# Kernel tuning notes

Hardware: AMD Instinct MI355X
Metric: run time of the kernel (lower is better)

Reference implementation:

```python
import jax, jax.numpy as jnp
import numpy as np
from jax import lax

C_OUT = 32   # out_capsules[0]
D_OUT = 8    # out_capsules[1]
ROUTING_ITERS = 3
EPS = 1e-8


def squash(s):
    # squash over capsule-channel axis c (dim 1 of B c d h w)
    n2 = jnp.sum(s * s, axis=1, keepdims=True)
    return s * (n2 / (1.0 + n2)) / jnp.sqrt(n2 + EPS)


def setup_inputs() -> dict:
    key = jax.random.key(0)
    k1, k2 = jax.random.split(key)
    x = jax.random.normal(k1, (8, 16, 8, 96, 96), dtype=jnp.float32)
    # torch Conv3d weight layout: (out_ch, in_ch, kD, kH, kW); scaled ~ kaiming-ish
    w_conv = jax.random.normal(k2, (C_OUT * D_OUT, 16, 1, 3, 3), dtype=jnp.float32) * 0.05
    return {"x": x, "w_conv": w_conv}


def reference(x, w_conv):
    # Conv3d, no bias, valid padding, stride 1, kernel (1,3,3)
    u = lax.conv_general_dilated(
        x, w_conv, window_strides=(1, 1, 1), padding='VALID',
        dimension_numbers=('NCDHW', 'OIDHW', 'NCDHW'))  # (B, c*d, D, h, w)
    B, _, D, h, w = u.shape
    # rearrange 'B (c d) D h w -> B c D d h w'
    u = u.reshape(B, C_OUT, D_OUT, D, h, w).transpose(0, 1, 3, 2, 4, 5)

    b = jnp.zeros((B, D, D_OUT, h, w), dtype=u.dtype)
    s = None
    for _ in range(ROUTING_ITERS):
        # softmax_3d: exp normalized over (d, h, w), keeping D
        e = jnp.exp(b)
        c = e / jnp.sum(e, axis=(2, 3, 4), keepdims=True)
        s = jnp.einsum('BDdhw,BcDdhw->Bcdhw', c, u)
        b = b + jnp.einsum('BcDdhw,Bcdhw->BDdhw', u, squash(s))
    return s
```

## Files before the change

### kernel.cpp

```cpp
#include <hip/hip_runtime.h>
#include <math.h>

#define CIN   16
#define DDEP  8
#define HIN   96
#define WIN   96
#define HOUT  94
#define WOUT  94
#define HW    (HOUT*WOUT)
#define CH    256
#define DCAP  8
#define KTOT  (CIN*9)
#define KTILES 5
#define APAD  168
#define EPSQ  1e-8f

#define B_ELEMS ((size_t)8*DDEP*DCAP*HW)
#define WFRAG_ELEMS ((size_t)KTILES*16*64*8)
#define BLK_PER_B (94*12)
#define NBLK ((size_t)8*BLK_PER_B)
#define A_TILE_BYTES ((size_t)64*APAD*2)
#define A_TILE_V4 (A_TILE_BYTES/16)
#define AC_BYTES (NBLK*A_TILE_BYTES)

typedef __attribute__((ext_vector_type(8))) short bf16x8;
typedef __attribute__((ext_vector_type(4))) float f32x4;

__device__ __forceinline__ ushort f2bf(float f) {
    unsigned u = __float_as_uint(f);
    return (ushort)((u + 0x7FFFu + ((u >> 16) & 1u)) >> 16);
}
__device__ __forceinline__ float bf2f(ushort h) {
    return __uint_as_float(((unsigned)h) << 16);
}

__global__ __launch_bounds__(64) void build_wfrag(
    const float* __restrict__ w, ushort* __restrict__ w_hi, ushort* __restrict__ w_lo)
{
    const int lane = threadIdx.x;
    const int nt = blockIdx.x, kt = blockIdx.y;
    const int n  = nt*16 + (lane & 15);
    const int kb = kt*32 + (lane >> 4)*8;
    size_t off = (((size_t)kt*16 + nt)*64 + lane)*8;
    for (int j = 0; j < 8; ++j) {
        int k = kb + j;
        float v = (k < KTOT) ? w[(size_t)n*KTOT + k] : 0.f;
        ushort hi = f2bf(v);
        float  r  = v - bf2f(hi);
        ushort lo = f2bf(r);
        w_hi[off + j] = hi; w_lo[off + j] = lo;
    }
}

__global__ __launch_bounds__(256) void zreduce(
    const float* __restrict__ Zp, float* __restrict__ Z, int dst)
{
    const int bd = blockIdx.x;
    const float* p = Zp + (size_t)bd * BLK_PER_B;
    float s = 0.f;
    for (int i = threadIdx.x; i < BLK_PER_B; i += 256) s += p[i];
    #pragma unroll
    for (int off = 1; off < 64; off <<= 1) s += __shfl_xor(s, off);
    __shared__ float ps[4];
    if ((threadIdx.x & 63) == 0) ps[threadIdx.x >> 6] = s;
    __syncthreads();
    if (threadIdx.x == 0) Z[dst + bd] = ps[0] + ps[1] + ps[2] + ps[3];
}

template<int MODE>
__device__ __forceinline__ void routing_epilogue(
    const f32x4 (&acc)[4][4], const int t, const int wx, const int h0, const int bb,
    const float (*cms)[8], const float* invZ,
    float (*n2s)[8][8], float (*dbs)[8][8][8], float (*sout)[8],
    float* __restrict__ bws, float* __restrict__ Zp, float* __restrict__ out)
{
    const int w0 = wx*8;
    const int wv = t >> 6, lane = t & 63;
    const int m16 = lane & 15, quad = lane >> 4;
    const int d   = m16 & 7;
    const int Dq  = quad >> 1;
    const int wih = quad & 1;

    float svv[4][4];
    {
        float cmw[4][4];
        if (MODE == 0) {
            const float inv = 1.0f / (float)(DCAP * HW);
            #pragma unroll
            for (int mt = 0; mt < 4; ++mt)
                #pragma unroll
                for (int r = 0; r < 4; ++r) cmw[mt][r] = inv;
        } else {
            #pragma unroll
            for (int mt = 0; mt < 4; ++mt) {
                int D = mt*2 + Dq;
                float iz = invZ[D];
                #pragma unroll
                for (int r = 0; r < 4; ++r) cmw[mt][r] = cms[D*8 + d][wih*4 + r] * iz;
            }
        }
        #pragma unroll
        for (int nt = 0; nt < 4; ++nt)
            #pragma unroll
            for (int r = 0; r < 4; ++r) {
                float partial = 0.f;
                #pragma unroll
                for (int mt = 0; mt < 4; ++mt) partial += cmw[mt][r]*acc[mt][nt][r];
                partial += __shfl_xor(partial, 32);
                svv[nt][r] = partial;
            }
    }

    if (MODE == 2) {
        if (quad < 2) {
            #pragma unroll
            for (int nt = 0; nt < 4; ++nt) {
                int ch = wv*64 + nt*16 + m16;
                #pragma unroll
                for (int r = 0; r < 4; ++r) sout[ch][wih*4 + r] = svv[nt][r];
            }
        }
        __syncthreads();
        for (int i = t; i < 1024; i += 256) {
            int c2 = i >> 2, wip = i & 3;
            int w = w0 + wip*2;
            if (w + 1 < WOUT) {
                float2 v2 = { sout[c2][wip*2], sout[c2][wip*2 + 1] };
                *(float2*)&out[((size_t)bb*CH + c2)*HW + (size_t)h0*WOUT + w] = v2;
            }
        }
        return;
    }

    float p2[4];
    #pragma unroll
    for (int r = 0; r < 4; ++r) {
        float s2 = 0.f;
        #pragma unroll
        for (int nt = 0; nt < 4; ++nt) s2 += svv[nt][r]*svv[nt][r];
        p2[r] = s2;
    }
    #pragma unroll
    for (int r = 0; r < 4; ++r) p2[r] += __shfl_xor(p2[r], 8);
    if (quad < 2 && m16 < 8) {
        #pragma unroll
        for (int r = 0; r < 4; ++r) n2s[wv][m16][quad*4 + r] = p2[r];
    }
    __syncthreads();
    float fac[4];
    #pragma unroll
    for (int r = 0; r < 4; ++r) {
        int wi = wih*4 + r;
        float n2 = n2s[0][d][wi] + n2s[1][d][wi] + n2s[2][d][wi] + n2s[3][d][wi];
        fac[r] = (n2 / (1.f + n2)) / sqrtf(n2 + EPSQ);
    }
    float qv[4][4];
    #pragma unroll
    for (int mt = 0; mt < 4; ++mt)
        #pragma unroll
        for (int r = 0; r < 4; ++r) {
            float sum = 0.f;
            #pragma unroll
            for (int nt = 0; nt < 4; ++nt)
                sum += acc[mt][nt][r] * (svv[nt][r] * fac[r]);
            qv[mt][r] = sum;
        }
    #pragma unroll
    for (int mt = 0; mt < 4; ++mt)
        #pragma unroll
        for (int r = 0; r < 4; ++r) qv[mt][r] += __shfl_xor(qv[mt][r], 8);
    if (m16 < 8) {
        #pragma unroll
        for (int mt = 0; mt < 4; ++mt) {
            int D = mt*2 + Dq;
            #pragma unroll
            for (int r = 0; r < 4; ++r) dbs[wv][D][m16][wih*4 + r] = qv[mt][r];
        }
    }
    __syncthreads();
    {
        int Dd = t >> 2, wip = t & 3;
        int D = Dd >> 3, d2 = Dd & 7;
        int w = w0 + wip*2;
        float ez = 0.f;
        if (w + 1 < WOUT) {
            int wi = wip*2;
            float2 add;
            add.x = dbs[0][D][d2][wi]   + dbs[1][D][d2][wi]
                  + dbs[2][D][d2][wi]   + dbs[3][D][d2][wi];
            add.y = dbs[0][D][d2][wi+1] + dbs[1][D][d2][wi+1]
                  + dbs[2][D][d2][wi+1] + dbs[3][D][d2][wi+1];
            float2* bp = (float2*)&bws[((size_t)bb*64 + Dd)*HW + (size_t)h0*WOUT + w];
            if (MODE != 0) { float2 old = *bp; add.x += old.x; add.y += old.y; }
            *bp = add;
            ez = expf(add.x) + expf(add.y);
        }
        #pragma unroll
        for (int off = 1; off < 32; off <<= 1) ez += __shfl_xor(ez, off);
        if ((t & 31) == 0)
            Zp[((size_t)bb*8 + D)*BLK_PER_B + h0*12 + wx] = ez;
    }
}

template<int MODE, int AC>
__global__ __launch_bounds__(256, 2) void conv_mfma_route(
    const float* __restrict__ x,
    const ushort* __restrict__ w_hi, const ushort* __restrict__ w_lo,
    float* __restrict__ bws, const float* __restrict__ Z,
    float* __restrict__ Zp, float* __restrict__ out, float* __restrict__ Ac)
{
    const int t  = threadIdx.x;
    const int wx = blockIdx.x, h0 = blockIdx.y, bb = blockIdx.z;
    const int w0 = wx*8;
    const size_t blk = ((size_t)bb*94 + h0)*12 + wx;

    __shared__ __align__(16) ushort a_hi[64][APAD];
    __shared__ float  cms[64][8];
    __shared__ float  invZ[8];
    __shared__ union {
        float patch[CIN][DDEP][3][10];
        struct { float n2s[4][8][8];
                 float dbs[4][8][8][8]; } ep;
        float sout[256][8];
    } ov;

    if (MODE != 0) {
        if (t < 8) invZ[t] = 1.0f / Z[(MODE == 2 ? 64 : 0) + bb*8 + t];
        for (int v = t; v < 512; v += 256) {
            int Dd = v >> 3, wi = v & 7;
            int w = w0 + wi;
            float bv = (w < WOUT) ? bws[((size_t)bb*64 + Dd)*HW + (size_t)h0*WOUT + w] : 0.f;
            cms[Dd][wi] = expf(bv);
        }
    }

    if (AC == 2) {
        const float4* src = (const float4*)Ac + blk*A_TILE_V4;
        float4* dst = (float4*)&a_hi[0][0];
        for (int i = t; i < A_TILE_V4; i += 256) dst[i] = src[i];
        __syncthreads();
    } else {
        for (int i = t; i < CIN*DDEP*3*10; i += 256) {
            int ci = i / 240, rem = i - ci*240;
            int D  = rem / 30, rem2 = rem - D*30;
            int kh = rem2 / 10, col = rem2 - kh*10;
            int xc = w0 + col; if (xc > 95) xc = 95;
            ov.patch[ci][D][kh][col] =
                x[(((size_t)(bb*CIN + ci)*DDEP + D)*HIN + (h0+kh))*WIN + xc];
        }
        __syncthreads();

        {
            const int site = t >> 2, kg = t & 3;
            const int D = site >> 3, wi = site & 7;
            #pragma unroll
            for (int u2 = 0; u2 < 18; ++u2) {
                int k0 = kg*36 + u2*2;
                int ci0 = k0/9, r0 = k0 - ci0*9, kh0 = r0/3, kw0 = r0 - kh0*3;
                int k1 = k0 + 1;
                int ci1 = k1/9, r1 = k1 - ci1*9, kh1 = r1/3, kw1 = r1 - kh1*3;
                unsigned lo = f2bf(ov.patch[ci0][D][kh0][wi+kw0]);
                unsigned hi = f2bf(ov.patch[ci1][D][kh1][wi+kw1]);
                *(unsigned*)&a_hi[site][k0] = lo | (hi << 16);
            }
            if (t < 64) {
                #pragma unroll
                for (int kk = KTOT; kk < KTILES*32; kk += 2)
                    *(unsigned*)&a_hi[t][kk] = 0u;
            }
        }
        __syncthreads();
    }

    const int wv = t >> 6, lane = t & 63;
    const int m16 = lane & 15, quad = lane >> 4;
    f32x4 acc[4][4];
    #pragma unroll
    for (int mt = 0; mt < 4; ++mt)
        #pragma unroll
        for (int nt = 0; nt < 4; ++nt)
            acc[mt][nt] = (f32x4){0.f, 0.f, 0.f, 0.f};

    #pragma unroll
    for (int kt = 0; kt < KTILES; ++kt) {
        bf16x8 ah[4];
        #pragma unroll
        for (int mt = 0; mt < 4; ++mt)
            ah[mt] = *(const bf16x8*)&a_hi[mt*16 + m16][kt*32 + quad*8];
        #pragma unroll
        for (int nt = 0; nt < 4; ++nt) {
            size_t off = (((size_t)kt*16 + (wv*4 + nt))*64 + lane)*8;
            bf16x8 bh = *(const bf16x8*)&w_hi[off];
            bf16x8 bl = *(const bf16x8*)&w_lo[off];
            #pragma unroll
            for (int mt = 0; mt < 4; ++mt) {
                acc[mt][nt] = __builtin_amdgcn_mfma_f32_16x16x32_bf16(ah[mt], bh, acc[mt][nt], 0, 0, 0);
                acc[mt][nt] = __builtin_amdgcn_mfma_f32_16x16x32_bf16(ah[mt], bl, acc[mt][nt], 0, 0, 0);
            }
        }
    }

    if (AC == 1) {
        float4* dst = (float4*)Ac + blk*A_TILE_V4;
        const float4* src = (const float4*)&a_hi[0][0];
        for (int i = t; i < A_TILE_V4; i += 256) dst[i] = src[i];
    }

    routing_epilogue<MODE>(acc, t, wx, h0, bb, cms, invZ,
                           ov.ep.n2s, ov.ep.dbs, ov.sout, bws, Zp, out);
}

extern "C" void kernel_launch(void* const* d_in, const int* in_sizes, int n_in,
                              void* d_out, int out_size, void* d_ws, size_t ws_size,
                              hipStream_t stream)
{
    (void)in_sizes; (void)n_in; (void)out_size;
    const float* x     = (const float*)d_in[0];
    const float* wconv = (const float*)d_in[1];
    float* out = (float*)d_out;

    float*  bws  = (float*)d_ws;
    float*  Z    = bws + B_ELEMS;
    float*  Zp   = Z + 128;
    ushort* w_hi = (ushort*)(Zp + 64*BLK_PER_B);
    ushort* w_lo = w_hi + WFRAG_ELEMS;
    size_t  base = (size_t)((char*)(w_lo + WFRAG_ELEMS) - (char*)d_ws);
    size_t  aoff = (base + 255) & ~(size_t)255;
    float*  Ac   = (float*)((char*)d_ws + aoff);
    const bool big = ws_size >= aoff + AC_BYTES;

    const dim3 grid(12, 94, 8);
    build_wfrag<<<dim3(16, KTILES), 64, 0, stream>>>(wconv, w_hi, w_lo);
    if (big) {
        conv_mfma_route<0, 1><<<grid, 256, 0, stream>>>(x, w_hi, w_lo, bws, Z, Zp, out, Ac);
        zreduce<<<64, 256, 0, stream>>>(Zp, Z, 0);
        conv_mfma_route<1, 2><<<grid, 256, 0, stream>>>(x, w_hi, w_lo, bws, Z, Zp, out, Ac);
        zreduce<<<64, 256, 0, stream>>>(Zp, Z, 64);
        conv_mfma_route<2, 2><<<grid, 256, 0, stream>>>(x, w_hi, w_lo, bws, Z, Zp, out, Ac);
    } else {
        conv_mfma_route<0, 0><<<grid, 256, 0, stream>>>(x, w_hi, w_lo, bws, Z, Zp, out, nullptr);
        zreduce<<<64, 256, 0, stream>>>(Zp, Z, 0);
        conv_mfma_route<1, 0><<<grid, 256, 0, stream>>>(x, w_hi, w_lo, bws, Z, Zp, out, nullptr);
        zreduce<<<64, 256, 0, stream>>>(Zp, Z, 64);
        conv_mfma_route<2, 0><<<grid, 256, 0, stream>>>(x, w_hi, w_lo, bws, Z, Zp, out, nullptr);
    }
}
```

Measured before the change: 595.0 us.

## Replace middle routing iteration with per-site Gram matrix of capsule predictions

```diff
diff --git a/kernel.cpp b/kernel.cpp
--- a/kernel.cpp
+++ b/kernel.cpp
@@ -22,6 +22,9 @@
 #define A_TILE_BYTES ((size_t)64*APAD*2)
 #define A_TILE_V4 (A_TILE_BYTES/16)
 #define AC_BYTES (NBLK*A_TILE_BYTES)
+#define VSITES (DCAP*HW)
+#define NBLK2  277
+#define G_BYTES ((size_t)8*VSITES*36*4)
 
 typedef __attribute__((ext_vector_type(8))) short bf16x8;
 typedef __attribute__((ext_vector_type(4))) float f32x4;
@@ -53,12 +56,12 @@
 }
 
 __global__ __launch_bounds__(256) void zreduce(
-    const float* __restrict__ Zp, float* __restrict__ Z, int dst)
+    const float* __restrict__ Zp, float* __restrict__ Z, int dst, int count)
 {
     const int bd = blockIdx.x;
-    const float* p = Zp + (size_t)bd * BLK_PER_B;
+    const float* p = Zp + (size_t)bd * count;
     float s = 0.f;
-    for (int i = threadIdx.x; i < BLK_PER_B; i += 256) s += p[i];
+    for (int i = threadIdx.x; i < count; i += 256) s += p[i];
     #pragma unroll
     for (int off = 1; off < 64; off <<= 1) s += __shfl_xor(s, off);
     __shared__ float ps[4];
@@ -202,12 +205,13 @@
     }
 }
 
-template<int MODE, int AC>
+template<int MODE, int AC, bool GW>
 __global__ __launch_bounds__(256, 2) void conv_mfma_route(
     const float* __restrict__ x,
     const ushort* __restrict__ w_hi, const ushort* __restrict__ w_lo,
     float* __restrict__ bws, const float* __restrict__ Z,
-    float* __restrict__ Zp, float* __restrict__ out, float* __restrict__ Ac)
+    float* __restrict__ Zp, float* __restrict__ out,
+    float* __restrict__ Ac, float* __restrict__ Gm)
 {
     const int t  = threadIdx.x;
     const int wx = blockIdx.x, h0 = blockIdx.y, bb = blockIdx.z;
@@ -222,6 +226,7 @@
         struct { float n2s[4][8][8];
                  float dbs[4][8][8][8]; } ep;
         float sout[256][8];
+        float gst[4][16][36];
     } ov;
 
     if (MODE != 0) {
@@ -274,6 +279,7 @@
 
     const int wv = t >> 6, lane = t & 63;
     const int m16 = lane & 15, quad = lane >> 4;
+    const int Dq = quad >> 1, wih = quad & 1;
     f32x4 acc[4][4];
     #pragma unroll
     for (int mt = 0; mt < 4; ++mt)
@@ -308,6 +314,127 @@
 
     routing_epilogue<MODE>(acc, t, wx, h0, bb, cms, invZ,
                            ov.ep.n2s, ov.ep.dbs, ov.sout, bws, Zp, out);
+
+    if constexpr (GW) {
+        const int c3 = m16 >> 3;
+        const int dL = m16 & 7;
+        __syncthreads();
+        #pragma unroll
+        for (int r = 0; r < 4; ++r) {
+            const int rq = r >> 1;
+            float G36[36];
+            #pragma unroll
+            for (int j = 0; j < 36; ++j) G36[j] = 0.f;
+            #pragma unroll
+            for (int nt = 0; nt < 4; ++nt) {
+                float u8[8];
+                #pragma unroll
+                for (int mt = 0; mt < 4; ++mt) {
+                    float own = acc[mt][nt][r];
+                    float oth = __shfl_xor(own, 32);
+                    if (Dq == 0) { u8[mt*2]   = own; u8[mt*2+1] = oth; }
+                    else         { u8[mt*2+1] = own; u8[mt*2]   = oth; }
+                }
+                if (Dq == rq) {
+                    int idx = 0;
+                    #pragma unroll
+                    for (int D = 0; D < 8; ++D)
+                        #pragma unroll
+                        for (int Dp = D; Dp < 8; ++Dp) {
+                            G36[idx] += u8[D]*u8[Dp];
+                            ++idx;
+                        }
+                }
+            }
+            if (Dq == rq) {
+                #pragma unroll
+                for (int j = 0; j < 36; ++j) G36[j] += __shfl_xor(G36[j], 8);
+                if (c3 == 0) {
+                    #pragma unroll
+                    for (int j = 0; j < 36; ++j) ov.gst[wv][dL*2 + wih][j] = G36[j];
+                }
+            }
+            __syncthreads();
+            for (int idx2 = t; idx2 < 16*36; idx2 += 256) {
+                int sidx = idx2 / 36, j = idx2 - sidx*36;
+                int dd = sidx >> 1, wh = sidx & 1;
+                int w = w0 + wh*4 + r;
+                if (w < WOUT) {
+                    float gv = ov.gst[0][sidx][j] + ov.gst[1][sidx][j]
+                             + ov.gst[2][sidx][j] + ov.gst[3][sidx][j];
+                    size_t gsite = ((size_t)(bb*DCAP + dd)*HOUT + h0)*WOUT + w;
+                    Gm[gsite*36 + j] = gv;
+                }
+            }
+            __syncthreads();
+        }
+    }
+}
+
+__global__ __launch_bounds__(256) void gram_route(
+    const float* __restrict__ Gm, float* __restrict__ bws,
+    const float* __restrict__ Z, float* __restrict__ Zp)
+{
+    const int k = blockIdx.x, bb = blockIdx.y;
+    const int t = threadIdx.x;
+    const int local = k*256 + t;
+    const bool valid = local < VSITES;
+    float ez[8];
+    #pragma unroll
+    for (int D = 0; D < 8; ++D) ez[D] = 0.f;
+    if (valid) {
+        const int d  = local / HW;
+        const int r2 = local - d*HW;
+        float bv[8], cm[8];
+        #pragma unroll
+        for (int D = 0; D < 8; ++D) {
+            bv[D] = bws[((size_t)(bb*64 + D*8 + d))*HW + r2];
+            cm[D] = expf(bv[D]) * (1.0f / Z[bb*8 + D]);
+        }
+        float g[36];
+        const float4* gp = (const float4*)(Gm + (size_t)(bb*VSITES + local)*36);
+        #pragma unroll
+        for (int q = 0; q < 9; ++q) {
+            float4 v = gp[q];
+            g[q*4+0] = v.x; g[q*4+1] = v.y; g[q*4+2] = v.z; g[q*4+3] = v.w;
+        }
+        float tD[8];
+        #pragma unroll
+        for (int D = 0; D < 8; ++D) tD[D] = 0.f;
+        {
+            int idx = 0;
+            #pragma unroll
+            for (int D = 0; D < 8; ++D)
+                #pragma unroll
+                for (int Dp = D; Dp < 8; ++Dp) {
+                    float gv = g[idx]; ++idx;
+                    tD[D] += cm[Dp] * gv;
+                    if (Dp != D) tD[Dp] += cm[D] * gv;
+                }
+        }
+        float n2 = 0.f;
+        #pragma unroll
+        for (int D = 0; D < 8; ++D) n2 += cm[D] * tD[D];
+        float fac = (n2 / (1.f + n2)) / sqrtf(n2 + EPSQ);
+        #pragma unroll
+        for (int D = 0; D < 8; ++D) {
+            float nb = bv[D] + fac * tD[D];
+            bws[((size_t)(bb*64 + D*8 + d))*HW + r2] = nb;
+            ez[D] = expf(nb);
+        }
+    }
+    #pragma unroll
+    for (int D = 0; D < 8; ++D)
+        #pragma unroll
+        for (int off = 1; off < 64; off <<= 1) ez[D] += __shfl_xor(ez[D], off);
+    __shared__ float ps[4][8];
+    if ((t & 63) == 0) {
+        #pragma unroll
+        for (int D = 0; D < 8; ++D) ps[t >> 6][D] = ez[D];
+    }
+    __syncthreads();
+    if (t < 8)
+        Zp[((size_t)bb*8 + t)*NBLK2 + k] = ps[0][t] + ps[1][t] + ps[2][t] + ps[3][t];
 }
 
 extern "C" void kernel_launch(void* const* d_in, const int* in_sizes, int n_in,
@@ -325,23 +452,32 @@
     ushort* w_hi = (ushort*)(Zp + 64*BLK_PER_B);
     ushort* w_lo = w_hi + WFRAG_ELEMS;
     size_t  base = (size_t)((char*)(w_lo + WFRAG_ELEMS) - (char*)d_ws);
-    size_t  aoff = (base + 255) & ~(size_t)255;
+    size_t  goff = (base + 255) & ~(size_t)255;
+    float*  Gm   = (float*)((char*)d_ws + goff);
+    size_t  aoff = (goff + G_BYTES + 255) & ~(size_t)255;
     float*  Ac   = (float*)((char*)d_ws + aoff);
-    const bool big = ws_size >= aoff + AC_BYTES;
+    const bool haveG = ws_size >= goff + G_BYTES;
+    const bool haveA = ws_size >= aoff + AC_BYTES;
 
     const dim3 grid(12, 94, 8);
     build_wfrag<<<dim3(16, KTILES), 64, 0, stream>>>(wconv, w_hi, w_lo);
-    if (big) {
-        conv_mfma_route<0, 1><<<grid, 256, 0, stream>>>(x, w_hi, w_lo, bws, Z, Zp, out, Ac);
-        zreduce<<<64, 256, 0, stream>>>(Zp, Z, 0);
-        conv_mfma_route<1, 2><<<grid, 256, 0, stream>>>(x, w_hi, w_lo, bws, Z, Zp, out, Ac);
-        zreduce<<<64, 256, 0, stream>>>(Zp, Z, 64);
-        conv_mfma_route<2, 2><<<grid, 256, 0, stream>>>(x, w_hi, w_lo, bws, Z, Zp, out, Ac);
+    if (haveG && haveA) {
+        conv_mfma_route<0, 1, true ><<<grid, 256, 0, stream>>>(x, w_hi, w_lo, bws, Z, Zp, out, Ac, Gm);
+        zreduce<<<64, 256, 0, stream>>>(Zp, Z, 0, BLK_PER_B);
+        gram_route<<<dim3(NBLK2, 8), 256, 0, stream>>>(Gm, bws, Z, Zp);
+        zreduce<<<64, 256, 0, stream>>>(Zp, Z, 64, NBLK2);
+        conv_mfma_route<2, 2, false><<<grid, 256, 0, stream>>>(x, w_hi, w_lo, bws, Z, Zp, out, Ac, nullptr);
+    } else if (haveG) {
+        conv_mfma_route<0, 0, true ><<<grid, 256, 0, stream>>>(x, w_hi, w_lo, bws, Z, Zp, out, nullptr, Gm);
+        zreduce<<<64, 256, 0, stream>>>(Zp, Z, 0, BLK_PER_B);
+        gram_route<<<dim3(NBLK2, 8), 256, 0, stream>>>(Gm, bws, Z, Zp);
+        zreduce<<<64, 256, 0, stream>>>(Zp, Z, 64, NBLK2);
+        conv_mfma_route<2, 0, false><<<grid, 256, 0, stream>>>(x, w_hi, w_lo, bws, Z, Zp, out, nullptr, nullptr);
     } else {
-        conv_mfma_route<0, 0><<<grid, 256, 0, stream>>>(x, w_hi, w_lo, bws, Z, Zp, out, nullptr);
-        zreduce<<<64, 256, 0, stream>>>(Zp, Z, 0);
-        conv_mfma_route<1, 0><<<grid, 256, 0, stream>>>(x, w_hi, w_lo, bws, Z, Zp, out, nullptr);
-        zreduce<<<64, 256, 0, stream>>>(Zp, Z, 64);
-        conv_mfma_route<2, 0><<<grid, 256, 0, stream>>>(x, w_hi, w_lo, bws, Z, Zp, out, nullptr);
-    }
-}
+        conv_mfma_route<0, 0, false><<<grid, 256, 0, stream>>>(x, w_hi, w_lo, bws, Z, Zp, out, nullptr, nullptr);
+        zreduce<<<64, 256, 0, stream>>>(Zp, Z, 0, BLK_PER_B);
+        conv_mfma_route<1, 0, false><<<grid, 256, 0, stream>>>(x, w_hi, w_lo, bws, Z, Zp, out, nullptr, nullptr);
+        zreduce<<<64, 256, 0, stream>>>(Zp, Z, 64, BLK_PER_B);
+        conv_mfma_route<2, 0, false><<<grid, 256, 0, stream>>>(x, w_hi, w_lo, bws, Z, Zp, out, nullptr, nullptr);
+    }
+}
```

Result: no change. 592.0 us (-0.5%).
